# Performance work log

Hardware: AMD Instinct MI355X
Metric: run time of the kernel (lower is better)

Reference implementation:

```python
import jax, jax.numpy as jnp
import numpy as np

DIM = 1024
HEADS = 16
HEAD_DIM = DIM // HEADS
B, S = 2, 2048


def setup_inputs() -> dict:
    key = jax.random.key(0)
    ks = jax.random.split(key, 10)
    sc = lambda fan_in: 1.0 / np.sqrt(fan_in)
    return {
        "x": jax.random.normal(ks[0], (B, S, 1), dtype=jnp.float32),
        "w_in": jax.random.uniform(ks[1], (1, DIM), jnp.float32, -1.0, 1.0),
        "b_in": jax.random.uniform(ks[2], (DIM,), jnp.float32, -1.0, 1.0),
        "wq": jax.random.uniform(ks[3], (DIM, DIM), jnp.float32, -sc(DIM), sc(DIM)),
        "wk": jax.random.uniform(ks[4], (DIM, DIM), jnp.float32, -sc(DIM), sc(DIM)),
        "wv": jax.random.uniform(ks[5], (DIM, DIM), jnp.float32, -sc(DIM), sc(DIM)),
        "wo": jax.random.uniform(ks[6], (DIM, DIM), jnp.float32, -sc(DIM), sc(DIM)),
        "bo": jax.random.uniform(ks[7], (DIM,), jnp.float32, -sc(DIM), sc(DIM)),
        "wf": jax.random.uniform(ks[8], (DIM, 1), jnp.float32, -sc(DIM), sc(DIM)),
        "bf": jax.random.uniform(ks[9], (1,), jnp.float32, -sc(DIM), sc(DIM)),
    }


def reference(x, w_in, b_in, wq, wk, wv, wo, bo, wf, bf):
    b, s, _ = x.shape
    scale = HEAD_DIM ** -0.5
    h = x @ w_in + b_in                      # [b, s, dim]
    q = (h @ wq).reshape(b, s, HEADS, HEAD_DIM)
    k = (h @ wk).reshape(b, s, HEADS, HEAD_DIM)
    v = (h @ wv).reshape(b, s, HEADS, HEAD_DIM)
    scores = jnp.einsum("bqhd,bkhd->bhqk", q, k) * scale  # [b, h, s, s]
    causal = jnp.triu(jnp.ones((s, s), dtype=bool), k=1)
    scores = jnp.where(causal, -jnp.inf, scores)
    attn = jax.nn.softmax(scores, axis=-1)   # dropout is identity in eval
    out = jnp.einsum("bhqk,bkhd->bqhd", attn, v).reshape(b, s, DIM)
    out = out @ wo + bo
    out = out @ wf + bf                      # [b, s, 1]
    return jnp.transpose(out, (0, 2, 1))     # [b, 1, s]
```

## Files before the change

### kernel.cpp

```cpp
#include <hip/hip_runtime.h>

#define DIM 1024
#define HEADS 16
#define BATCH 2
#define SEQ 2048
#define NTERM 32

#define WS_P0   0
#define WS_P1   5120
#define WS_U    10240
#define WS_T    16384

__global__ __launch_bounds__(256) void k1_weights(
        const float* __restrict__ x,
        const float* __restrict__ w_in, const float* __restrict__ b_in,
        const float* __restrict__ wq,   const float* __restrict__ wk,
        const float* __restrict__ wv,   const float* __restrict__ wo,
        const float* __restrict__ wf,   float* __restrict__ ws) {
    const int bid = blockIdx.x;
    const int tid = threadIdx.x;
    if (bid < 192) {
        const int m  = bid >> 6;
        const int r  = bid & 63;
        const int jh = r & 1;
        const int d0 = (r >> 1) * 32;
        const int dl = tid & 7;
        const int jg = tid >> 3;
        const int j0 = jh * 512 + jg * 16;
        const float* Wm = (m == 0) ? wq : (m == 1) ? wk : wv;
        float4 a1 = {0, 0, 0, 0}, a2 = {0, 0, 0, 0};
        #pragma unroll
        for (int i = 0; i < 16; ++i) {
            const int j = j0 + i;
            const float4 v = *reinterpret_cast<const float4*>(Wm + j * DIM + d0 + 4 * dl);
            const float wi = w_in[j];
            a1.x += wi * v.x; a1.y += wi * v.y; a1.z += wi * v.z; a1.w += wi * v.w;
            if (m != 1) {
                const float bi = b_in[j];
                a2.x += bi * v.x; a2.y += bi * v.y; a2.z += bi * v.z; a2.w += bi * v.w;
            }
        }
        __shared__ float sh1[32][33], sh2[32][33];
        sh1[jg][4 * dl + 0] = a1.x;
        sh1[jg][4 * dl + 1] = a1.y;
        sh1[jg][4 * dl + 2] = a1.z;
        sh1[jg][4 * dl + 3] = a1.w;
        if (m != 1) {
            sh2[jg][4 * dl + 0] = a2.x;
            sh2[jg][4 * dl + 1] = a2.y;
            sh2[jg][4 * dl + 2] = a2.z;
            sh2[jg][4 * dl + 3] = a2.w;
        }
        __syncthreads();
        if (tid < 32) {
            float f1 = 0.f, f2 = 0.f;
            #pragma unroll
            for (int g = 0; g < 32; ++g) {
                f1 += sh1[g][tid];
                if (m != 1) f2 += sh2[g][tid];
            }
            const int base = jh ? WS_P1 : WS_P0;
            const int d = d0 + tid;
            if (m == 0)      { ws[base + d] = f1; ws[base + 1024 + d] = f2; }
            else if (m == 1) { ws[base + 2048 + d] = f1; }
            else             { ws[base + 3072 + d] = f1; ws[base + 4096 + d] = f2; }
        }
    } else if (bid < 256) {
        const int wave = tid >> 6, lane = tid & 63;
        const int rb = bid - 192;
        #pragma unroll
        for (int rr = 0; rr < 4; ++rr) {
            const int row = rb * 16 + wave * 4 + rr;
            const float4* wo4 = reinterpret_cast<const float4*>(wo + row * DIM);
            const float4* wf4 = reinterpret_cast<const float4*>(wf);
            float s = 0.f;
            #pragma unroll
            for (int e = lane; e < 256; e += 64) {
                const float4 a = wo4[e], b = wf4[e];
                s += a.x * b.x + a.y * b.y + a.z * b.z + a.w * b.w;
            }
            #pragma unroll
            for (int off = 32; off; off >>= 1) s += __shfl_down(s, off);
            if (lane == 0) ws[WS_U + row] = s;
        }
    } else {
        const int sb = bid - 256;
        const int b = sb >> 5, n = sb & 31;
        const float* xb = x + b * SEQ;
        const float4 xa = ((const float4*)xb)[2 * tid];
        const float4 xc = ((const float4*)xb)[2 * tid + 1];
        float xv[8] = {xa.x, xa.y, xa.z, xa.w, xc.x, xc.y, xc.z, xc.w};
        float pw[8];
        #pragma unroll
        for (int e = 0; e < 8; ++e) pw[e] = 1.f;
        float f = 1.f;
        for (int i = 1; i <= n; ++i) {
            f *= (float)i;
            #pragma unroll
            for (int e = 0; e < 8; ++e) pw[e] *= xv[e];
        }
        const float rf = 1.0f / f;
        float p[8];
        float s = 0.f;
        #pragma unroll
        for (int e = 0; e < 8; ++e) { s += pw[e] * rf; p[e] = s; }
        const int lane = tid & 63, wv = tid >> 6;
        float incl = s;
        #pragma unroll
        for (int off = 1; off < 64; off <<= 1) {
            const float v = __shfl_up(incl, off);
            if (lane >= off) incl += v;
        }
        __shared__ float wsum[4];
        if (lane == 63) wsum[wv] = incl;
        __syncthreads();
        float base = incl - s;
        if (wv > 0) base += wsum[0];
        if (wv > 1) base += wsum[1];
        if (wv > 2) base += wsum[2];
        float* Trow = ws + WS_T + (b * NTERM + n) * SEQ;
        ((float4*)Trow)[2 * tid]     = make_float4(base + p[0], base + p[1], base + p[2], base + p[3]);
        ((float4*)Trow)[2 * tid + 1] = make_float4(base + p[4], base + p[5], base + p[6], base + p[7]);
    }
}

__global__ __launch_bounds__(256) void k2_eval(
        const float* __restrict__ x,  const float* __restrict__ bo,
        const float* __restrict__ wf, const float* __restrict__ bf,
        const float* __restrict__ ws, float* __restrict__ out) {
    const int tid = threadIdx.x;
    const int wave = tid >> 6, lane = tid & 63;

    __shared__ float sA[HEADS], sC[HEADS], sG[HEADS];
    __shared__ float c0p[4];

    #pragma unroll
    for (int hh = 0; hh < 4; ++hh) {
        const int h = wave * 4 + hh;
        const int d = h * 64 + lane;
        const float qa = ws[WS_P0 + d]        + ws[WS_P1 + d];
        const float qb = ws[WS_P0 + 1024 + d] + ws[WS_P1 + 1024 + d];
        const float ka = ws[WS_P0 + 2048 + d] + ws[WS_P1 + 2048 + d];
        const float va = ws[WS_P0 + 3072 + d] + ws[WS_P1 + 3072 + d];
        const float u  = ws[WS_U + d];
        float pA = qa * ka, pC = qb * ka, pG = va * u;
        #pragma unroll
        for (int off = 32; off; off >>= 1) {
            pA += __shfl_down(pA, off);
            pC += __shfl_down(pC, off);
            pG += __shfl_down(pG, off);
        }
        if (lane == 0) { sA[h] = pA; sC[h] = pC; sG[h] = pG; }
    }
    {
        float s = 0.f;
        #pragma unroll
        for (int t = 0; t < 4; ++t) {
            const int d = wave * 256 + t * 64 + lane;
            const float vb = ws[WS_P0 + 4096 + d] + ws[WS_P1 + 4096 + d];
            s += vb * ws[WS_U + d] + bo[d] * wf[d];
        }
        #pragma unroll
        for (int off = 32; off; off >>= 1) s += __shfl_down(s, off);
        if (lane == 0) c0p[wave] = s;
    }
    __syncthreads();
    const float c0 = c0p[0] + c0p[1] + c0p[2] + c0p[3] + bf[0];

    const int g = blockIdx.x * 256 + tid;
    const int h = g & 15;
    const int q = (g >> 4) & (SEQ - 1);
    const int b = g >> 15;
    const float xq = x[b * SEQ + q];
    const float al = 0.125f * (sA[h] * xq + sC[h]);
    const float* T = ws + WS_T + b * NTERM * SEQ + q;
    float tr[NTERM];
    #pragma unroll
    for (int n = 0; n < NTERM; ++n) tr[n] = T[n * SEQ];
    float den = tr[31];
    float num = 31.f * tr[31];
    #pragma unroll
    for (int j = 30; j >= 1; --j) {
        den = den * al + tr[j];
        num = num * al + (float)j * tr[j];
    }
    den = den * al + tr[0];
    float r = sG[h] * (num / den);
    r += __shfl_down(r, 8);
    r += __shfl_down(r, 4);
    r += __shfl_down(r, 2);
    r += __shfl_down(r, 1);
    if (h == 0) out[b * SEQ + q] = c0 + r;
}

extern "C" void kernel_launch(void* const* d_in, const int* in_sizes, int n_in,
                              void* d_out, int out_size, void* d_ws, size_t ws_size,
                              hipStream_t stream) {
    const float* x    = (const float*)d_in[0];
    const float* w_in = (const float*)d_in[1];
    const float* b_in = (const float*)d_in[2];
    const float* wq   = (const float*)d_in[3];
    const float* wk   = (const float*)d_in[4];
    const float* wv   = (const float*)d_in[5];
    const float* wo   = (const float*)d_in[6];
    const float* bo   = (const float*)d_in[7];
    const float* wf   = (const float*)d_in[8];
    const float* bf   = (const float*)d_in[9];
    float* out = (float*)d_out;
    float* ws  = (float*)d_ws;

    k1_weights<<<320, 256, 0, stream>>>(x, w_in, b_in, wq, wk, wv, wo, wf, ws);
    k2_eval<<<256, 256, 0, stream>>>(x, bo, wf, bf, ws, out);
}
```

Before: 16.15 us.

## Split weight reduction four ways and transpose Taylor table to per-query rows

The weight-folding stage now splits the 1024-long reduction into four quarters instead of two, which doubles the block count for the matrix-vector part and raises parallelism, at the cost of more partial sums for the eval kernel to add. The Taylor prefix-sum table is stored query-major, with 32 terms contiguous per query, so each eval thread loads its terms with eight float4 reads instead of 32 strided scalar loads. The k1 table writes become strided scattered stores, which may cost write bandwidth.

```diff
diff --git a/kernel.cpp b/kernel.cpp
--- a/kernel.cpp
+++ b/kernel.cpp
@@ -6,10 +6,9 @@
 #define SEQ 2048
 #define NTERM 32
 
-#define WS_P0   0
-#define WS_P1   5120
-#define WS_U    10240
-#define WS_T    16384
+#define WS_P    0
+#define WS_U    20480
+#define WS_T    24576
 
 __global__ __launch_bounds__(256) void k1_weights(
         const float* __restrict__ x,
@@ -19,18 +18,18 @@
         const float* __restrict__ wf,   float* __restrict__ ws) {
     const int bid = blockIdx.x;
     const int tid = threadIdx.x;
-    if (bid < 192) {
-        const int m  = bid >> 6;
-        const int r  = bid & 63;
-        const int jh = r & 1;
-        const int d0 = (r >> 1) * 32;
+    if (bid < 384) {
+        const int m  = bid >> 7;
+        const int r  = bid & 127;
+        const int jq = r & 3;
+        const int d0 = (r >> 2) * 32;
         const int dl = tid & 7;
         const int jg = tid >> 3;
-        const int j0 = jh * 512 + jg * 16;
+        const int j0 = jq * 256 + jg * 8;
         const float* Wm = (m == 0) ? wq : (m == 1) ? wk : wv;
         float4 a1 = {0, 0, 0, 0}, a2 = {0, 0, 0, 0};
         #pragma unroll
-        for (int i = 0; i < 16; ++i) {
+        for (int i = 0; i < 8; ++i) {
             const int j = j0 + i;
             const float4 v = *reinterpret_cast<const float4*>(Wm + j * DIM + d0 + 4 * dl);
             const float wi = w_in[j];
@@ -59,15 +58,15 @@
                 f1 += sh1[g][tid];
                 if (m != 1) f2 += sh2[g][tid];
             }
-            const int base = jh ? WS_P1 : WS_P0;
+            const int base = WS_P + jq * 5120;
             const int d = d0 + tid;
             if (m == 0)      { ws[base + d] = f1; ws[base + 1024 + d] = f2; }
             else if (m == 1) { ws[base + 2048 + d] = f1; }
             else             { ws[base + 3072 + d] = f1; ws[base + 4096 + d] = f2; }
         }
-    } else if (bid < 256) {
+    } else if (bid < 448) {
         const int wave = tid >> 6, lane = tid & 63;
-        const int rb = bid - 192;
+        const int rb = bid - 384;
         #pragma unroll
         for (int rr = 0; rr < 4; ++rr) {
             const int row = rb * 16 + wave * 4 + rr;
@@ -84,7 +83,7 @@
             if (lane == 0) ws[WS_U + row] = s;
         }
     } else {
-        const int sb = bid - 256;
+        const int sb = bid - 448;
         const int b = sb >> 5, n = sb & 31;
         const float* xb = x + b * SEQ;
         const float4 xa = ((const float4*)xb)[2 * tid];
@@ -118,9 +117,11 @@
         if (wv > 0) base += wsum[0];
         if (wv > 1) base += wsum[1];
         if (wv > 2) base += wsum[2];
-        float* Trow = ws + WS_T + (b * NTERM + n) * SEQ;
-        ((float4*)Trow)[2 * tid]     = make_float4(base + p[0], base + p[1], base + p[2], base + p[3]);
-        ((float4*)Trow)[2 * tid + 1] = make_float4(base + p[4], base + p[5], base + p[6], base + p[7]);
+        #pragma unroll
+        for (int e = 0; e < 8; ++e) {
+            const int q = tid * 8 + e;
+            ws[WS_T + (b * SEQ + q) * NTERM + n] = base + p[e];
+        }
     }
 }
 
@@ -138,11 +139,16 @@
     for (int hh = 0; hh < 4; ++hh) {
         const int h = wave * 4 + hh;
         const int d = h * 64 + lane;
-        const float qa = ws[WS_P0 + d]        + ws[WS_P1 + d];
-        const float qb = ws[WS_P0 + 1024 + d] + ws[WS_P1 + 1024 + d];
-        const float ka = ws[WS_P0 + 2048 + d] + ws[WS_P1 + 2048 + d];
-        const float va = ws[WS_P0 + 3072 + d] + ws[WS_P1 + 3072 + d];
-        const float u  = ws[WS_U + d];
+        float qa = 0.f, qb = 0.f, ka = 0.f, va = 0.f;
+        #pragma unroll
+        for (int jq = 0; jq < 4; ++jq) {
+            const float* P = ws + WS_P + jq * 5120 + d;
+            qa += P[0];
+            qb += P[1024];
+            ka += P[2048];
+            va += P[3072];
+        }
+        const float u = ws[WS_U + d];
         float pA = qa * ka, pC = qb * ka, pG = va * u;
         #pragma unroll
         for (int off = 32; off; off >>= 1) {
@@ -157,7 +163,9 @@
         #pragma unroll
         for (int t = 0; t < 4; ++t) {
             const int d = wave * 256 + t * 64 + lane;
-            const float vb = ws[WS_P0 + 4096 + d] + ws[WS_P1 + 4096 + d];
+            float vb = 0.f;
+            #pragma unroll
+            for (int jq = 0; jq < 4; ++jq) vb += ws[WS_P + jq * 5120 + 4096 + d];
             s += vb * ws[WS_U + d] + bo[d] * wf[d];
         }
         #pragma unroll
@@ -173,10 +181,16 @@
     const int b = g >> 15;
     const float xq = x[b * SEQ + q];
     const float al = 0.125f * (sA[h] * xq + sC[h]);
-    const float* T = ws + WS_T + b * NTERM * SEQ + q;
+    const float4* T4 = reinterpret_cast<const float4*>(ws + WS_T + (b * SEQ + q) * NTERM);
     float tr[NTERM];
     #pragma unroll
-    for (int n = 0; n < NTERM; ++n) tr[n] = T[n * SEQ];
+    for (int i = 0; i < 8; ++i) {
+        const float4 v = T4[i];
+        tr[4 * i + 0] = v.x;
+        tr[4 * i + 1] = v.y;
+        tr[4 * i + 2] = v.z;
+        tr[4 * i + 3] = v.w;
+    }
     float den = tr[31];
     float num = 31.f * tr[31];
     #pragma unroll
@@ -209,6 +223,6 @@
     float* out = (float*)d_out;
     float* ws  = (float*)d_ws;
 
-    k1_weights<<<320, 256, 0, stream>>>(x, w_in, b_in, wq, wk, wv, wo, wf, ws);
+    k1_weights<<<512, 256, 0, stream>>>(x, w_in, b_in, wq, wk, wv, wo, wf, ws);
     k2_eval<<<256, 256, 0, stream>>>(x, bo, wf, bf, ws, out);
 }
```

Measured after the change: 16.57 us. +2.6%, slower.
